# Kernel optimization log

Measured on AMD Instinct MI355X. Metric: run time of the kernel, lower is better.

## Reference

```python
import jax, jax.numpy as jnp
import numpy as np

CODEBOOK_SIZE = 1024
EMB_DIM = 64


def setup_inputs() -> dict:
    key = jax.random.key(0)
    k1, k2 = jax.random.split(key)
    z = jax.random.normal(k1, (4, EMB_DIM, 32, 32, 32), dtype=jnp.float32)
    embedding = jax.random.normal(k2, (CODEBOOK_SIZE, EMB_DIM), dtype=jnp.float32)
    return {"z": z, "embedding": embedding}


def reference(z, embedding):
    # z: [b, c, h, w, d], embedding: [K, c]
    b, c, h, w, d = z.shape
    K = embedding.shape[0]
    # flatten to [N, c] with channels last (matches permute(0,2,3,4,1).reshape)
    zf = jnp.transpose(z, (0, 2, 3, 4, 1)).reshape(-1, c)
    # squared L2 distance to each codebook entry: ||z||^2 - 2 z.e + ||e||^2
    dist = (
        jnp.sum(zf * zf, axis=1, keepdims=True)
        - 2.0 * zf @ embedding.T
        + jnp.sum(embedding * embedding, axis=1)[None, :]
    )  # [N, K]
    min_encoding_indices = jnp.argmin(dist, axis=1)  # [N]
    # one-hot @ embedding == gather (same math, no NxK materialization)
    z_q = embedding[min_encoding_indices]  # [N, c]
    z_q = jnp.transpose(z_q.reshape(b, h, w, d, c), (0, 4, 1, 2, 3))
    # straight-through estimator
    z_q = z + jax.lax.stop_gradient(z_q - z)
    # perplexity from mean one-hot occupancy
    n_tokens = zf.shape[0]
    e_mean = jnp.bincount(min_encoding_indices, length=K).astype(zf.dtype) / n_tokens
    perplexity = jnp.exp(-jnp.sum(e_mean * jnp.log(e_mean + 1e-10)))
    loss = jnp.asarray(0.0, dtype=z.dtype)
    return (
        z_q,
        loss,
        perplexity,
        min_encoding_indices.reshape(b, h, w, d),
        jnp.mean(dist),
    )
```

## Files before the change

kernel.cpp:

```cpp
#include <hip/hip_runtime.h>

#define CH     64
#define KC     1024
#define SP     32768
#define NBATCH 4
#define NTOK   (NBATCH * SP)
#define MTOK   64
#define SZZ    68
#define ECH    128
#define NCHK   (KC / ECH)
#define CAP    16
#define MARGIN 3.0f

#define OFF_ZQ   0
#define OFF_LOSS (NBATCH * CH * SP)
#define OFF_PERP (OFF_LOSS + 1)
#define OFF_IDX  (OFF_PERP + 1)
#define OFF_MEAN (OFF_IDX + NTOK)


typedef __attribute__((ext_vector_type(8))) short  s16x8;
typedef __attribute__((ext_vector_type(4))) float  f32x4;

__device__ __forceinline__ unsigned short f2bf(float f) {
    unsigned int u = __float_as_uint(f);
    return (unsigned short)((u + 0x7fffu + ((u >> 16) & 1u)) >> 16);
}

__device__ __forceinline__ float exact_dist(const float* zrow,
                                            const float* __restrict__ emb,
                                            const float* __restrict__ enl, int c) {
    const float4* er = (const float4*)(emb + (size_t)c * CH);
    float a0 = 0.f, a1 = 0.f, a2 = 0.f, a3 = 0.f;
#pragma unroll
    for (int j = 0; j < 16; ++j) {
        float4 e4 = er[j];
        a0 = fmaf(zrow[4 * j + 0], e4.x, a0);
        a1 = fmaf(zrow[4 * j + 1], e4.y, a1);
        a2 = fmaf(zrow[4 * j + 2], e4.z, a2);
        a3 = fmaf(zrow[4 * j + 3], e4.w, a3);
    }
    return enl[c] - 2.f * ((a0 + a1) + (a2 + a3));
}

__global__ __launch_bounds__(256) void prep(const float* __restrict__ e,
                                            int* __restrict__ hist,
                                            float* __restrict__ sums,
                                            float* __restrict__ sum_zc,
                                            float* __restrict__ sum_ec,
                                            float* __restrict__ enorm,
                                            unsigned short* __restrict__ eb) {
    const int tid = threadIdx.x;
    const int bk = blockIdx.x;
    if (bk < 4) {
        int k = bk * 256 + tid;
        const float4* row = (const float4*)(e + (size_t)k * CH);
        float n = 0.f;
#pragma unroll
        for (int j = 0; j < CH / 4; ++j) {
            float4 v = row[j];
            n += v.x * v.x + v.y * v.y + v.z * v.z + v.w * v.w;
        }
        enorm[k] = n;
    } else if (bk == 4) {
        if (tid == 0) sums[0] = 0.f;
        if (tid < 64) sum_zc[tid] = 0.f;
        __shared__ float ls1[256];
        __shared__ float r2[4];
        int c = tid & 63;
        int strip = tid >> 6;
        float s1 = 0.f, s2 = 0.f;
        for (int k = strip * 256; k < strip * 256 + 256; ++k) {
            float v = e[k * CH + c];
            s1 += v;
            s2 = fmaf(v, v, s2);
        }
        ls1[tid] = s1;
        for (int off = 32; off; off >>= 1) s2 += __shfl_down(s2, off);
        if ((tid & 63) == 0) r2[tid >> 6] = s2;
        __syncthreads();
        if (strip == 0) sum_ec[c] = ls1[c] + ls1[64 + c] + ls1[128 + c] + ls1[192 + c];
        if (tid == 0) sums[1] = r2[0] + r2[1] + r2[2] + r2[3];
    } else if (bk < 9) {
        hist[(bk - 5) * 256 + tid] = 0;
    } else {
        int base = (bk - 9) * 16384;
        for (int j = 0; j < 64; ++j) {
            int i = base + tid + j * 256;
            eb[i] = f2bf(e[i]);
        }
    }
}

#define GLD16(gsrc, ldst)                                                        \
    __builtin_amdgcn_global_load_lds(                                            \
        (const __attribute__((address_space(1))) unsigned int*)(gsrc),           \
        (__attribute__((address_space(3))) unsigned int*)(ldst), 16, 0, 0)

__global__ __launch_bounds__(256, 2) void vq_main(const float* __restrict__ z,
                                                  const float* __restrict__ emb,
                                                  const unsigned short* __restrict__ eb,
                                                  const float* __restrict__ enorm,
                                                  float* __restrict__ out,
                                                  int* __restrict__ hist,
                                                  float* __restrict__ sums,
                                                  float* __restrict__ sum_zc) {
    __shared__ float zl[MTOK * SZZ];
    __shared__ __align__(16) unsigned short ebl[ECH * 64];
    __shared__ float enl[ECH];
    __shared__ int   cand[MTOK][CAP];
    __shared__ int   ccnt[MTOK];
    __shared__ int   fi[MTOK];
    __shared__ float rbest[4][MTOK];
    __shared__ int   rbi[4][MTOK];

    const int tid = threadIdx.x;
    const int w = tid >> 6;
    const int lane = tid & 63;
    const int n15 = lane & 15;
    const int q = lane >> 4;
    const int t0 = blockIdx.x * MTOK;
    const int bb = t0 >> 15;
    const int s0 = t0 & (SP - 1);

    const int l3 = lane >> 3, l7 = lane & 7;
    const size_t gofs = (size_t)((l7 ^ l3) << 3);
#define STAGE(cb)                                                             \
    {                                                                         \
        _Pragma("unroll")                                                     \
        for (int it = 0; it < 4; ++it) {                                      \
            const unsigned short* gs =                                        \
                eb + (size_t)((cb) + (w << 5) + it * 8 + l3) * CH + gofs;     \
            GLD16(gs, (char*)ebl + (w << 12) + (it << 10));                   \
        }                                                                     \
    }

    {
        const float* zbase = z + ((size_t)bb * CH) * SP + s0;
#pragma unroll
        for (int j = 0; j < 4; ++j) {
            int idx = tid + j * 256;
            int c = idx >> 4;
            int tq = idx & 15;
            float4 v = *(const float4*)(zbase + (size_t)c * SP + tq * 4);
            zl[(4 * tq + 0) * SZZ + c] = v.x;
            zl[(4 * tq + 1) * SZZ + c] = v.y;
            zl[(4 * tq + 2) * SZZ + c] = v.z;
            zl[(4 * tq + 3) * SZZ + c] = v.w;
        }
        if (tid < MTOK) ccnt[tid] = 0;
    }
    __syncthreads();

    s16x8 A0, A1;
    {
        const float* zrow = &zl[(w * 16 + n15) * SZZ];
        float4 za = *(const float4*)(zrow + q * 8);
        float4 zb = *(const float4*)(zrow + q * 8 + 4);
        float4 zc = *(const float4*)(zrow + 32 + q * 8);
        float4 zd = *(const float4*)(zrow + 32 + q * 8 + 4);
        A0[0] = (short)f2bf(za.x); A0[1] = (short)f2bf(za.y);
        A0[2] = (short)f2bf(za.z); A0[3] = (short)f2bf(za.w);
        A0[4] = (short)f2bf(zb.x); A0[5] = (short)f2bf(zb.y);
        A0[6] = (short)f2bf(zb.z); A0[7] = (short)f2bf(zb.w);
        A1[0] = (short)f2bf(zc.x); A1[1] = (short)f2bf(zc.y);
        A1[2] = (short)f2bf(zc.z); A1[3] = (short)f2bf(zc.w);
        A1[4] = (short)f2bf(zd.x); A1[5] = (short)f2bf(zd.y);
        A1[6] = (short)f2bf(zd.z); A1[7] = (short)f2bf(zd.w);
    }
    const int gsw = q ^ (n15 & 7);

    float bmin[4] = {3.4e38f, 3.4e38f, 3.4e38f, 3.4e38f};
    for (int ch = 0; ch < NCHK; ++ch) {
        __syncthreads();
        STAGE(ch * ECH)
        if (tid < ECH) enl[tid] = enorm[ch * ECH + tid];
        __syncthreads();
        for (int ct = 0; ct < ECH / 16; ++ct) {
            const s16x8* rowp = (const s16x8*)&ebl[(size_t)(ct * 16 + n15) << 6];
            s16x8 B0 = rowp[gsw];
            s16x8 B1 = rowp[gsw ^ 4];
            f32x4 acc = {0.f, 0.f, 0.f, 0.f};
            acc = __builtin_amdgcn_mfma_f32_16x16x32_bf16(A0, B0, acc, 0, 0, 0);
            acc = __builtin_amdgcn_mfma_f32_16x16x32_bf16(A1, B1, acc, 0, 0, 0);
            float en = enl[ct * 16 + n15];
#pragma unroll
            for (int r = 0; r < 4; ++r) {
                float d = fmaf(-2.f, acc[r], en);
                bmin[r] = fminf(bmin[r], d);
            }
        }
    }
#pragma unroll
    for (int off = 1; off < 16; off <<= 1)
#pragma unroll
        for (int r = 0; r < 4; ++r)
            bmin[r] = fminf(bmin[r], __shfl_xor(bmin[r], off));
    float thr[4];
#pragma unroll
    for (int r = 0; r < 4; ++r) thr[r] = bmin[r] + MARGIN;

    for (int cc = 0; cc < NCHK; ++cc) {
        int ch = (cc == 0) ? (NCHK - 1) : (cc - 1);
        if (cc) {
            __syncthreads();
            STAGE(ch * ECH)
            if (tid < ECH) enl[tid] = enorm[ch * ECH + tid];
            __syncthreads();
        }
        for (int ct = 0; ct < ECH / 16; ++ct) {
            const s16x8* rowp = (const s16x8*)&ebl[(size_t)(ct * 16 + n15) << 6];
            s16x8 B0 = rowp[gsw];
            s16x8 B1 = rowp[gsw ^ 4];
            f32x4 acc = {0.f, 0.f, 0.f, 0.f};
            acc = __builtin_amdgcn_mfma_f32_16x16x32_bf16(A0, B0, acc, 0, 0, 0);
            acc = __builtin_amdgcn_mfma_f32_16x16x32_bf16(A1, B1, acc, 0, 0, 0);
            float en = enl[ct * 16 + n15];
#pragma unroll
            for (int r = 0; r < 4; ++r) {
                float d = fmaf(-2.f, acc[r], en);
                if (d <= thr[r]) {
                    int t = w * 16 + 4 * q + r;
                    int pos = atomicAdd(&ccnt[t], 1);
                    if (pos < CAP) cand[t][pos] = ch * ECH + ct * 16 + n15;
                }
            }
        }
    }
    __syncthreads();

    {
        const int t = tid & 63;
        const int part = tid >> 6;
        const float* zrow = &zl[t * SZZ];
        int cnt = ccnt[t];
        float best = 3.4e38f;
        int bi = 0;
        if (cnt <= CAP) {
            for (int j = part; j < cnt; j += 4) {
                int c = cand[t][j];
                float d = exact_dist(zrow, emb, enorm, c);
                if (d < best || (d == best && c < bi)) { best = d; bi = c; }
            }
        } else {
            for (int c = part; c < KC; c += 4) {
                float d = exact_dist(zrow, emb, enorm, c);
                if (d < best || (d == best && c < bi)) { best = d; bi = c; }
            }
        }
        rbest[part][t] = best;
        rbi[part][t] = bi;
    }
    __syncthreads();
    if (tid < MTOK) {
        float best = rbest[0][tid];
        int bi = rbi[0][tid];
#pragma unroll
        for (int p = 1; p < 4; ++p) {
            float b = rbest[p][tid];
            int i = rbi[p][tid];
            if (b < best || (b == best && i < bi)) { best = b; bi = i; }
        }
        fi[tid] = bi;
        out[OFF_IDX + t0 + tid] = (float)bi;
        atomicAdd(&hist[bi], 1);
    }
    __syncthreads();

#pragma unroll
    for (int j = 0; j < 16; ++j) {
        int idx = tid + j * 256;
        int c = idx >> 6;
        int t = idx & 63;
        int code = fi[t];
        float ev = emb[(size_t)code * CH + c];
        float zv = zl[t * SZZ + c];
        out[OFF_ZQ + ((size_t)bb * CH + c) * SP + s0 + t] = zv + (ev - zv);
    }

    {
        float* zs1 = reinterpret_cast<float*>(cand);
        float* zs2 = zs1 + 256;
        int c = tid >> 2, qq = tid & 3;
        float s1 = 0.f, s2 = 0.f;
        for (int tt = 0; tt < 16; ++tt) {
            float v = zl[(qq * 16 + tt) * SZZ + c];
            s1 += v;
            s2 = fmaf(v, v, s2);
        }
        zs1[tid] = s1;
        zs2[tid] = s2;
        __syncthreads();
        if (tid < 64) {
            float a = zs1[4 * tid] + zs1[4 * tid + 1] + zs1[4 * tid + 2] + zs1[4 * tid + 3];
            atomicAdd(&sum_zc[tid], a);
            float bsum = zs2[4 * tid] + zs2[4 * tid + 1] + zs2[4 * tid + 2] + zs2[4 * tid + 3];
            for (int off = 32; off; off >>= 1) bsum += __shfl_down(bsum, off);
            if (tid == 0) atomicAdd(&sums[0], bsum);
        }
    }
#undef STAGE
}

__global__ __launch_bounds__(1024) void finalize(const int* __restrict__ hist,
                                                 const float* __restrict__ sums,
                                                 const float* __restrict__ sum_zc,
                                                 const float* __restrict__ sum_ec,
                                                 float* __restrict__ out) {
    __shared__ float red[1024];
    int k = threadIdx.x;
    float p = (float)hist[k] * (1.0f / (float)NTOK);
    red[k] = p * logf(p + 1e-10f);
    __syncthreads();
    for (int off = 512; off; off >>= 1) {
        if (k < off) red[k] += red[k + off];
        __syncthreads();
    }
    if (k == 0) {
        out[OFF_PERP] = expf(-red[0]);
        out[OFF_LOSS] = 0.f;
        double dot = 0.0;
        for (int c = 0; c < CH; ++c) dot += (double)sum_zc[c] * (double)sum_ec[c];
        double mean = ((double)KC * (double)sums[0] + (double)NTOK * (double)sums[1] - 2.0 * dot)
                      / ((double)NTOK * (double)KC);
        out[OFF_MEAN] = (float)mean;
    }
}

extern "C" void kernel_launch(void* const* d_in, const int* in_sizes, int n_in,
                              void* d_out, int out_size, void* d_ws, size_t ws_size,
                              hipStream_t stream) {
    const float* z   = (const float*)d_in[0];
    const float* emb = (const float*)d_in[1];
    float* out = (float*)d_out;

    int*            hist   = (int*)d_ws;
    float*          sums   = (float*)d_ws + 1024;
    float*          sum_zc = (float*)d_ws + 1026;
    float*          sum_ec = (float*)d_ws + 1090;
    float*          enorm  = (float*)d_ws + 1154;
    unsigned short* eb     = (unsigned short*)((int*)d_ws + 4096);

    prep<<<13, 256, 0, stream>>>(emb, hist, sums, sum_zc, sum_ec, enorm, eb);
    vq_main<<<NTOK / MTOK, 256, 0, stream>>>(z, emb, eb, enorm, out, hist, sums, sum_zc);
    finalize<<<1, 1024, 0, stream>>>(hist, sums, sum_zc, sum_ec, out);
}
```

Before: 209.8 us.

## Split codebook columns across waves, each wave covering all 64 tokens

Before, each wave held one 16-token A fragment and swept all 128 codes of each staged chunk. Now each wave holds A fragments for all 64 tokens and handles only its own 32-code slice, so every B fragment read from LDS feeds four MFMA pairs. Per-wave minima are merged through shared memory with an extra barrier to form the thresholds. This trades more A registers and a cross-wave reduction for fewer LDS B reads per MFMA.

```diff
diff --git a/kernel.cpp b/kernel.cpp
--- a/kernel.cpp
+++ b/kernel.cpp
@@ -96,6 +96,16 @@
     __builtin_amdgcn_global_load_lds(                                            \
         (const __attribute__((address_space(1))) unsigned int*)(gsrc),           \
         (__attribute__((address_space(3))) unsigned int*)(ldst), 16, 0, 0)
+
+#define MK8(A, ptr)                                            \
+    {                                                          \
+        float4 _a = *(const float4*)(ptr);                     \
+        float4 _b = *(const float4*)((ptr) + 4);               \
+        A[0] = (short)f2bf(_a.x); A[1] = (short)f2bf(_a.y);    \
+        A[2] = (short)f2bf(_a.z); A[3] = (short)f2bf(_a.w);    \
+        A[4] = (short)f2bf(_b.x); A[5] = (short)f2bf(_b.y);    \
+        A[6] = (short)f2bf(_b.z); A[7] = (short)f2bf(_b.w);    \
+    }
 
 __global__ __launch_bounds__(256, 2) void vq_main(const float* __restrict__ z,
                                                   const float* __restrict__ emb,
@@ -152,53 +162,85 @@
     }
     __syncthreads();
 
-    s16x8 A0, A1;
+    s16x8 A00, A01, A10, A11, A20, A21, A30, A31;
     {
-        const float* zrow = &zl[(w * 16 + n15) * SZZ];
-        float4 za = *(const float4*)(zrow + q * 8);
-        float4 zb = *(const float4*)(zrow + q * 8 + 4);
-        float4 zc = *(const float4*)(zrow + 32 + q * 8);
-        float4 zd = *(const float4*)(zrow + 32 + q * 8 + 4);
-        A0[0] = (short)f2bf(za.x); A0[1] = (short)f2bf(za.y);
-        A0[2] = (short)f2bf(za.z); A0[3] = (short)f2bf(za.w);
-        A0[4] = (short)f2bf(zb.x); A0[5] = (short)f2bf(zb.y);
-        A0[6] = (short)f2bf(zb.z); A0[7] = (short)f2bf(zb.w);
-        A1[0] = (short)f2bf(zc.x); A1[1] = (short)f2bf(zc.y);
-        A1[2] = (short)f2bf(zc.z); A1[3] = (short)f2bf(zc.w);
-        A1[4] = (short)f2bf(zd.x); A1[5] = (short)f2bf(zd.y);
-        A1[6] = (short)f2bf(zd.z); A1[7] = (short)f2bf(zd.w);
+        const float* zr0 = &zl[(0 * 16 + n15) * SZZ];
+        const float* zr1 = &zl[(1 * 16 + n15) * SZZ];
+        const float* zr2 = &zl[(2 * 16 + n15) * SZZ];
+        const float* zr3 = &zl[(3 * 16 + n15) * SZZ];
+        MK8(A00, zr0 + q * 8) MK8(A01, zr0 + 32 + q * 8)
+        MK8(A10, zr1 + q * 8) MK8(A11, zr1 + 32 + q * 8)
+        MK8(A20, zr2 + q * 8) MK8(A21, zr2 + 32 + q * 8)
+        MK8(A30, zr3 + q * 8) MK8(A31, zr3 + 32 + q * 8)
     }
     const int gsw = q ^ (n15 & 7);
 
-    float bmin[4] = {3.4e38f, 3.4e38f, 3.4e38f, 3.4e38f};
+    float bm0[4] = {3.4e38f, 3.4e38f, 3.4e38f, 3.4e38f};
+    float bm1[4] = {3.4e38f, 3.4e38f, 3.4e38f, 3.4e38f};
+    float bm2[4] = {3.4e38f, 3.4e38f, 3.4e38f, 3.4e38f};
+    float bm3[4] = {3.4e38f, 3.4e38f, 3.4e38f, 3.4e38f};
     for (int ch = 0; ch < NCHK; ++ch) {
         __syncthreads();
         STAGE(ch * ECH)
         if (tid < ECH) enl[tid] = enorm[ch * ECH + tid];
         __syncthreads();
-        for (int ct = 0; ct < ECH / 16; ++ct) {
-            const s16x8* rowp = (const s16x8*)&ebl[(size_t)(ct * 16 + n15) << 6];
+#pragma unroll
+        for (int ct = 0; ct < 2; ++ct) {
+            const int row = (w << 5) + ct * 16 + n15;
+            const s16x8* rowp = (const s16x8*)&ebl[(size_t)row << 6];
             s16x8 B0 = rowp[gsw];
             s16x8 B1 = rowp[gsw ^ 4];
-            f32x4 acc = {0.f, 0.f, 0.f, 0.f};
-            acc = __builtin_amdgcn_mfma_f32_16x16x32_bf16(A0, B0, acc, 0, 0, 0);
-            acc = __builtin_amdgcn_mfma_f32_16x16x32_bf16(A1, B1, acc, 0, 0, 0);
-            float en = enl[ct * 16 + n15];
+            float en = enl[row];
+            f32x4 a0 = {0.f, 0.f, 0.f, 0.f};
+            f32x4 a1 = {0.f, 0.f, 0.f, 0.f};
+            f32x4 a2 = {0.f, 0.f, 0.f, 0.f};
+            f32x4 a3 = {0.f, 0.f, 0.f, 0.f};
+            a0 = __builtin_amdgcn_mfma_f32_16x16x32_bf16(A00, B0, a0, 0, 0, 0);
+            a0 = __builtin_amdgcn_mfma_f32_16x16x32_bf16(A01, B1, a0, 0, 0, 0);
+            a1 = __builtin_amdgcn_mfma_f32_16x16x32_bf16(A10, B0, a1, 0, 0, 0);
+            a1 = __builtin_amdgcn_mfma_f32_16x16x32_bf16(A11, B1, a1, 0, 0, 0);
+            a2 = __builtin_amdgcn_mfma_f32_16x16x32_bf16(A20, B0, a2, 0, 0, 0);
+            a2 = __builtin_amdgcn_mfma_f32_16x16x32_bf16(A21, B1, a2, 0, 0, 0);
+            a3 = __builtin_amdgcn_mfma_f32_16x16x32_bf16(A30, B0, a3, 0, 0, 0);
+            a3 = __builtin_amdgcn_mfma_f32_16x16x32_bf16(A31, B1, a3, 0, 0, 0);
 #pragma unroll
             for (int r = 0; r < 4; ++r) {
-                float d = fmaf(-2.f, acc[r], en);
-                bmin[r] = fminf(bmin[r], d);
+                bm0[r] = fminf(bm0[r], fmaf(-2.f, a0[r], en));
+                bm1[r] = fminf(bm1[r], fmaf(-2.f, a1[r], en));
+                bm2[r] = fminf(bm2[r], fmaf(-2.f, a2[r], en));
+                bm3[r] = fminf(bm3[r], fmaf(-2.f, a3[r], en));
             }
         }
     }
 #pragma unroll
     for (int off = 1; off < 16; off <<= 1)
 #pragma unroll
-        for (int r = 0; r < 4; ++r)
-            bmin[r] = fminf(bmin[r], __shfl_xor(bmin[r], off));
-    float thr[4];
-#pragma unroll
-    for (int r = 0; r < 4; ++r) thr[r] = bmin[r] + MARGIN;
+        for (int r = 0; r < 4; ++r) {
+            bm0[r] = fminf(bm0[r], __shfl_xor(bm0[r], off));
+            bm1[r] = fminf(bm1[r], __shfl_xor(bm1[r], off));
+            bm2[r] = fminf(bm2[r], __shfl_xor(bm2[r], off));
+            bm3[r] = fminf(bm3[r], __shfl_xor(bm3[r], off));
+        }
+    float* wmin = &rbest[0][0];
+    if (n15 == 0) {
+#pragma unroll
+        for (int r = 0; r < 4; ++r) {
+            wmin[w * 64 + 0 + 4 * q + r]  = bm0[r];
+            wmin[w * 64 + 16 + 4 * q + r] = bm1[r];
+            wmin[w * 64 + 32 + 4 * q + r] = bm2[r];
+            wmin[w * 64 + 48 + 4 * q + r] = bm3[r];
+        }
+    }
+    __syncthreads();
+    float thr0[4], thr1[4], thr2[4], thr3[4];
+#pragma unroll
+    for (int r = 0; r < 4; ++r) {
+        int i0 = 0 + 4 * q + r, i1 = 16 + 4 * q + r, i2 = 32 + 4 * q + r, i3 = 48 + 4 * q + r;
+        thr0[r] = fminf(fminf(wmin[i0], wmin[64 + i0]), fminf(wmin[128 + i0], wmin[192 + i0])) + MARGIN;
+        thr1[r] = fminf(fminf(wmin[i1], wmin[64 + i1]), fminf(wmin[128 + i1], wmin[192 + i1])) + MARGIN;
+        thr2[r] = fminf(fminf(wmin[i2], wmin[64 + i2]), fminf(wmin[128 + i2], wmin[192 + i2])) + MARGIN;
+        thr3[r] = fminf(fminf(wmin[i3], wmin[64 + i3]), fminf(wmin[128 + i3], wmin[192 + i3])) + MARGIN;
+    }
 
     for (int cc = 0; cc < NCHK; ++cc) {
         int ch = (cc == 0) ? (NCHK - 1) : (cc - 1);
@@ -208,21 +250,51 @@
             if (tid < ECH) enl[tid] = enorm[ch * ECH + tid];
             __syncthreads();
         }
-        for (int ct = 0; ct < ECH / 16; ++ct) {
-            const s16x8* rowp = (const s16x8*)&ebl[(size_t)(ct * 16 + n15) << 6];
+#pragma unroll
+        for (int ct = 0; ct < 2; ++ct) {
+            const int row = (w << 5) + ct * 16 + n15;
+            const s16x8* rowp = (const s16x8*)&ebl[(size_t)row << 6];
             s16x8 B0 = rowp[gsw];
             s16x8 B1 = rowp[gsw ^ 4];
-            f32x4 acc = {0.f, 0.f, 0.f, 0.f};
-            acc = __builtin_amdgcn_mfma_f32_16x16x32_bf16(A0, B0, acc, 0, 0, 0);
-            acc = __builtin_amdgcn_mfma_f32_16x16x32_bf16(A1, B1, acc, 0, 0, 0);
-            float en = enl[ct * 16 + n15];
+            float en = enl[row];
+            f32x4 a0 = {0.f, 0.f, 0.f, 0.f};
+            f32x4 a1 = {0.f, 0.f, 0.f, 0.f};
+            f32x4 a2 = {0.f, 0.f, 0.f, 0.f};
+            f32x4 a3 = {0.f, 0.f, 0.f, 0.f};
+            a0 = __builtin_amdgcn_mfma_f32_16x16x32_bf16(A00, B0, a0, 0, 0, 0);
+            a0 = __builtin_amdgcn_mfma_f32_16x16x32_bf16(A01, B1, a0, 0, 0, 0);
+            a1 = __builtin_amdgcn_mfma_f32_16x16x32_bf16(A10, B0, a1, 0, 0, 0);
+            a1 = __builtin_amdgcn_mfma_f32_16x16x32_bf16(A11, B1, a1, 0, 0, 0);
+            a2 = __builtin_amdgcn_mfma_f32_16x16x32_bf16(A20, B0, a2, 0, 0, 0);
+            a2 = __builtin_amdgcn_mfma_f32_16x16x32_bf16(A21, B1, a2, 0, 0, 0);
+            a3 = __builtin_amdgcn_mfma_f32_16x16x32_bf16(A30, B0, a3, 0, 0, 0);
+            a3 = __builtin_amdgcn_mfma_f32_16x16x32_bf16(A31, B1, a3, 0, 0, 0);
+            int code = ch * ECH + row;
 #pragma unroll
             for (int r = 0; r < 4; ++r) {
-                float d = fmaf(-2.f, acc[r], en);
-                if (d <= thr[r]) {
-                    int t = w * 16 + 4 * q + r;
+                float d0 = fmaf(-2.f, a0[r], en);
+                if (d0 <= thr0[r]) {
+                    int t = 0 + 4 * q + r;
                     int pos = atomicAdd(&ccnt[t], 1);
-                    if (pos < CAP) cand[t][pos] = ch * ECH + ct * 16 + n15;
+                    if (pos < CAP) cand[t][pos] = code;
+                }
+                float d1 = fmaf(-2.f, a1[r], en);
+                if (d1 <= thr1[r]) {
+                    int t = 16 + 4 * q + r;
+                    int pos = atomicAdd(&ccnt[t], 1);
+                    if (pos < CAP) cand[t][pos] = code;
+                }
+                float d2 = fmaf(-2.f, a2[r], en);
+                if (d2 <= thr2[r]) {
+                    int t = 32 + 4 * q + r;
+                    int pos = atomicAdd(&ccnt[t], 1);
+                    if (pos < CAP) cand[t][pos] = code;
+                }
+                float d3 = fmaf(-2.f, a3[r], en);
+                if (d3 <= thr3[r]) {
+                    int t = 48 + 4 * q + r;
+                    int pos = atomicAdd(&ccnt[t], 1);
+                    if (pos < CAP) cand[t][pos] = code;
                 }
             }
         }
```

Result: no change. 212.5 us (+1.3%).

## Double-buffer codebook chunk staging to overlap loads with MFMA compute

Applied to the files above, without the earlier changes.

Shrinks each codebook chunk from 128 to 64 entries and splits the LDS staging buffers into two halves. The next chunk's async global-to-LDS copy and norm load are issued before the current chunk is computed, in both the min-distance pass and the candidate pass. This hides global-load latency behind the MFMA work and cuts the barriers per chunk from two to one. The trade-off is twice as many chunk iterations, and correctness now depends on the barrier also waiting for the outstanding LDS-DMA loads.

```diff
diff --git a/kernel.cpp b/kernel.cpp
--- a/kernel.cpp
+++ b/kernel.cpp
@@ -7,7 +7,7 @@
 #define NTOK   (NBATCH * SP)
 #define MTOK   64
 #define SZZ    68
-#define ECH    128
+#define ECH    64
 #define NCHK   (KC / ECH)
 #define CAP    16
 #define MARGIN 3.0f
@@ -106,8 +106,8 @@
                                                   float* __restrict__ sums,
                                                   float* __restrict__ sum_zc) {
     __shared__ float zl[MTOK * SZZ];
-    __shared__ __align__(16) unsigned short ebl[ECH * 64];
-    __shared__ float enl[ECH];
+    __shared__ __align__(16) unsigned short ebl[2][ECH * 64];
+    __shared__ float enl[2][ECH];
     __shared__ int   cand[MTOK][CAP];
     __shared__ int   ccnt[MTOK];
     __shared__ int   fi[MTOK];
@@ -125,13 +125,13 @@
 
     const int l3 = lane >> 3, l7 = lane & 7;
     const size_t gofs = (size_t)((l7 ^ l3) << 3);
-#define STAGE(cb)                                                             \
+#define STAGE(cb, b)                                                          \
     {                                                                         \
         _Pragma("unroll")                                                     \
-        for (int it = 0; it < 4; ++it) {                                      \
+        for (int it = 0; it < 2; ++it) {                                      \
             const unsigned short* gs =                                        \
-                eb + (size_t)((cb) + (w << 5) + it * 8 + l3) * CH + gofs;     \
-            GLD16(gs, (char*)ebl + (w << 12) + (it << 10));                   \
+                eb + (size_t)((cb) + (w << 4) + it * 8 + l3) * CH + gofs;     \
+            GLD16(gs, (char*)ebl + (b) * 8192 + (w << 11) + (it << 10));      \
         }                                                                     \
     }
 
@@ -149,6 +149,8 @@
             zl[(4 * tq + 3) * SZZ + c] = v.w;
         }
         if (tid < MTOK) ccnt[tid] = 0;
+        STAGE(0, 0)
+        if (tid < ECH) enl[0][tid] = enorm[tid];
     }
     __syncthreads();
 
@@ -171,25 +173,29 @@
     const int gsw = q ^ (n15 & 7);
 
     float bmin[4] = {3.4e38f, 3.4e38f, 3.4e38f, 3.4e38f};
+    int buf = 0;
     for (int ch = 0; ch < NCHK; ++ch) {
-        __syncthreads();
-        STAGE(ch * ECH)
-        if (tid < ECH) enl[tid] = enorm[ch * ECH + tid];
-        __syncthreads();
+        if (ch < NCHK - 1) {
+            STAGE((ch + 1) * ECH, buf ^ 1)
+            if (tid < ECH) enl[buf ^ 1][tid] = enorm[(ch + 1) * ECH + tid];
+        }
+#pragma unroll
         for (int ct = 0; ct < ECH / 16; ++ct) {
-            const s16x8* rowp = (const s16x8*)&ebl[(size_t)(ct * 16 + n15) << 6];
+            const s16x8* rowp = (const s16x8*)&ebl[buf][(size_t)(ct * 16 + n15) << 6];
             s16x8 B0 = rowp[gsw];
             s16x8 B1 = rowp[gsw ^ 4];
             f32x4 acc = {0.f, 0.f, 0.f, 0.f};
             acc = __builtin_amdgcn_mfma_f32_16x16x32_bf16(A0, B0, acc, 0, 0, 0);
             acc = __builtin_amdgcn_mfma_f32_16x16x32_bf16(A1, B1, acc, 0, 0, 0);
-            float en = enl[ct * 16 + n15];
+            float en = enl[buf][ct * 16 + n15];
 #pragma unroll
             for (int r = 0; r < 4; ++r) {
                 float d = fmaf(-2.f, acc[r], en);
                 bmin[r] = fminf(bmin[r], d);
             }
         }
+        __syncthreads();
+        if (ch < NCHK - 1) buf ^= 1;
     }
 #pragma unroll
     for (int off = 1; off < 16; off <<= 1)
@@ -201,21 +207,20 @@
     for (int r = 0; r < 4; ++r) thr[r] = bmin[r] + MARGIN;
 
     for (int cc = 0; cc < NCHK; ++cc) {
-        int ch = (cc == 0) ? (NCHK - 1) : (cc - 1);
-        if (cc) {
-            __syncthreads();
-            STAGE(ch * ECH)
-            if (tid < ECH) enl[tid] = enorm[ch * ECH + tid];
-            __syncthreads();
-        }
+        const int ch = (cc == 0) ? (NCHK - 1) : (cc - 1);
+        if (cc < NCHK - 1) {
+            STAGE(cc * ECH, buf ^ 1)
+            if (tid < ECH) enl[buf ^ 1][tid] = enorm[cc * ECH + tid];
+        }
+#pragma unroll
         for (int ct = 0; ct < ECH / 16; ++ct) {
-            const s16x8* rowp = (const s16x8*)&ebl[(size_t)(ct * 16 + n15) << 6];
+            const s16x8* rowp = (const s16x8*)&ebl[buf][(size_t)(ct * 16 + n15) << 6];
             s16x8 B0 = rowp[gsw];
             s16x8 B1 = rowp[gsw ^ 4];
             f32x4 acc = {0.f, 0.f, 0.f, 0.f};
             acc = __builtin_amdgcn_mfma_f32_16x16x32_bf16(A0, B0, acc, 0, 0, 0);
             acc = __builtin_amdgcn_mfma_f32_16x16x32_bf16(A1, B1, acc, 0, 0, 0);
-            float en = enl[ct * 16 + n15];
+            float en = enl[buf][ct * 16 + n15];
 #pragma unroll
             for (int r = 0; r < 4; ++r) {
                 float d = fmaf(-2.f, acc[r], en);
@@ -226,8 +231,9 @@
                 }
             }
         }
-    }
-    __syncthreads();
+        __syncthreads();
+        if (cc < NCHK - 1) buf ^= 1;
+    }
 
     {
         const int t = tid & 63;
```

After: 218.2 us. +4.0%, slower.

## Keep whole bf16 codebook resident in LDS with persistent blocks over token tiles

Applied to the files above, without the earlier changes.

The kernel becomes persistent: 256 blocks each load the full 1024x64 bf16 codebook and the norms into about 159 KB of dynamic shared memory once, then loop over 8 token tiles. This removes the per-tile restaging of codebook chunks and the many barriers that went with each chunk, and the second pass no longer reloads chunks. In exchange occupancy falls to one 4-wave block per CU, so there is no overlap between global z loads, MFMA work and the refinement phase.

```diff
diff --git a/kernel.cpp b/kernel.cpp
--- a/kernel.cpp
+++ b/kernel.cpp
@@ -7,10 +7,20 @@
 #define NTOK   (NBATCH * SP)
 #define MTOK   64
 #define SZZ    68
-#define ECH    128
-#define NCHK   (KC / ECH)
+#define NBLK   256
+#define TILES  (NTOK / MTOK / NBLK)
 #define CAP    16
 #define MARGIN 3.0f
+
+#define OFF_EBL   0
+#define OFF_ZL    131072
+#define OFF_ENL   148480
+#define OFF_RBEST 152576
+#define OFF_RBI   153600
+#define OFF_CAND  154624
+#define OFF_CCNT  158720
+#define OFF_FI    158976
+#define SMEM_BYTES 159232
 
 #define OFF_ZQ   0
 #define OFF_LOSS (NBATCH * CH * SP)
@@ -97,86 +107,84 @@
         (const __attribute__((address_space(1))) unsigned int*)(gsrc),           \
         (__attribute__((address_space(3))) unsigned int*)(ldst), 16, 0, 0)
 
-__global__ __launch_bounds__(256, 2) void vq_main(const float* __restrict__ z,
-                                                  const float* __restrict__ emb,
-                                                  const unsigned short* __restrict__ eb,
-                                                  const float* __restrict__ enorm,
-                                                  float* __restrict__ out,
-                                                  int* __restrict__ hist,
-                                                  float* __restrict__ sums,
-                                                  float* __restrict__ sum_zc) {
-    __shared__ float zl[MTOK * SZZ];
-    __shared__ __align__(16) unsigned short ebl[ECH * 64];
-    __shared__ float enl[ECH];
-    __shared__ int   cand[MTOK][CAP];
-    __shared__ int   ccnt[MTOK];
-    __shared__ int   fi[MTOK];
-    __shared__ float rbest[4][MTOK];
-    __shared__ int   rbi[4][MTOK];
+__global__ __launch_bounds__(256) void vq_main(const float* __restrict__ z,
+                                               const float* __restrict__ emb,
+                                               const unsigned short* __restrict__ eb,
+                                               const float* __restrict__ enorm,
+                                               float* __restrict__ out,
+                                               int* __restrict__ hist,
+                                               float* __restrict__ sums,
+                                               float* __restrict__ sum_zc) {
+    extern __shared__ __align__(16) char smem[];
+    unsigned short* ebl = (unsigned short*)(smem + OFF_EBL);
+    float* zl   = (float*)(smem + OFF_ZL);
+    float* enl  = (float*)(smem + OFF_ENL);
+    float* rbest = (float*)(smem + OFF_RBEST);
+    int*   rbi   = (int*)(smem + OFF_RBI);
+    int (*cand)[CAP] = (int (*)[CAP])(smem + OFF_CAND);
+    int*   ccnt = (int*)(smem + OFF_CCNT);
+    int*   fi   = (int*)(smem + OFF_FI);
 
     const int tid = threadIdx.x;
     const int w = tid >> 6;
     const int lane = tid & 63;
     const int n15 = lane & 15;
     const int q = lane >> 4;
-    const int t0 = blockIdx.x * MTOK;
-    const int bb = t0 >> 15;
-    const int s0 = t0 & (SP - 1);
-
-    const int l3 = lane >> 3, l7 = lane & 7;
-    const size_t gofs = (size_t)((l7 ^ l3) << 3);
-#define STAGE(cb)                                                             \
-    {                                                                         \
-        _Pragma("unroll")                                                     \
-        for (int it = 0; it < 4; ++it) {                                      \
-            const unsigned short* gs =                                        \
-                eb + (size_t)((cb) + (w << 5) + it * 8 + l3) * CH + gofs;     \
-            GLD16(gs, (char*)ebl + (w << 12) + (it << 10));                   \
-        }                                                                     \
-    }
+    const int gsw = q ^ (n15 & 7);
 
     {
-        const float* zbase = z + ((size_t)bb * CH) * SP + s0;
-#pragma unroll
-        for (int j = 0; j < 4; ++j) {
-            int idx = tid + j * 256;
-            int c = idx >> 4;
-            int tq = idx & 15;
-            float4 v = *(const float4*)(zbase + (size_t)c * SP + tq * 4);
-            zl[(4 * tq + 0) * SZZ + c] = v.x;
-            zl[(4 * tq + 1) * SZZ + c] = v.y;
-            zl[(4 * tq + 2) * SZZ + c] = v.z;
-            zl[(4 * tq + 3) * SZZ + c] = v.w;
-        }
-        if (tid < MTOK) ccnt[tid] = 0;
-    }
-    __syncthreads();
-
-    s16x8 A0, A1;
-    {
-        const float* zrow = &zl[(w * 16 + n15) * SZZ];
-        float4 za = *(const float4*)(zrow + q * 8);
-        float4 zb = *(const float4*)(zrow + q * 8 + 4);
-        float4 zc = *(const float4*)(zrow + 32 + q * 8);
-        float4 zd = *(const float4*)(zrow + 32 + q * 8 + 4);
-        A0[0] = (short)f2bf(za.x); A0[1] = (short)f2bf(za.y);
-        A0[2] = (short)f2bf(za.z); A0[3] = (short)f2bf(za.w);
-        A0[4] = (short)f2bf(zb.x); A0[5] = (short)f2bf(zb.y);
-        A0[6] = (short)f2bf(zb.z); A0[7] = (short)f2bf(zb.w);
-        A1[0] = (short)f2bf(zc.x); A1[1] = (short)f2bf(zc.y);
-        A1[2] = (short)f2bf(zc.z); A1[3] = (short)f2bf(zc.w);
-        A1[4] = (short)f2bf(zd.x); A1[5] = (short)f2bf(zd.y);
-        A1[6] = (short)f2bf(zd.z); A1[7] = (short)f2bf(zd.w);
-    }
-    const int gsw = q ^ (n15 & 7);
-
-    float bmin[4] = {3.4e38f, 3.4e38f, 3.4e38f, 3.4e38f};
-    for (int ch = 0; ch < NCHK; ++ch) {
-        __syncthreads();
-        STAGE(ch * ECH)
-        if (tid < ECH) enl[tid] = enorm[ch * ECH + tid];
-        __syncthreads();
-        for (int ct = 0; ct < ECH / 16; ++ct) {
+        const int l3 = lane >> 3, l7 = lane & 7;
+        const size_t gofs = (size_t)((l7 ^ l3) << 3);
+        for (int it = 0; it < 32; ++it) {
+            const unsigned short* gs =
+                eb + (size_t)((w << 8) + it * 8 + l3) * CH + gofs;
+            GLD16(gs, (char*)ebl + (w << 15) + (it << 10));
+        }
+#pragma unroll
+        for (int j = 0; j < 4; ++j) enl[tid + j * 256] = enorm[tid + j * 256];
+    }
+
+    for (int tile = 0; tile < TILES; ++tile) {
+        const int t0 = (blockIdx.x + (tile << 8)) * MTOK;
+        const int bb = t0 >> 15;
+        const int s0 = t0 & (SP - 1);
+
+        {
+            const float* zbase = z + ((size_t)bb * CH) * SP + s0;
+#pragma unroll
+            for (int j = 0; j < 4; ++j) {
+                int idx = tid + j * 256;
+                int c = idx >> 4;
+                int tq = idx & 15;
+                float4 v = *(const float4*)(zbase + (size_t)c * SP + tq * 4);
+                zl[(4 * tq + 0) * SZZ + c] = v.x;
+                zl[(4 * tq + 1) * SZZ + c] = v.y;
+                zl[(4 * tq + 2) * SZZ + c] = v.z;
+                zl[(4 * tq + 3) * SZZ + c] = v.w;
+            }
+            if (tid < MTOK) ccnt[tid] = 0;
+        }
+        __syncthreads();
+
+        s16x8 A0, A1;
+        {
+            const float* zrow = &zl[(w * 16 + n15) * SZZ];
+            float4 za = *(const float4*)(zrow + q * 8);
+            float4 zb = *(const float4*)(zrow + q * 8 + 4);
+            float4 zc = *(const float4*)(zrow + 32 + q * 8);
+            float4 zd = *(const float4*)(zrow + 32 + q * 8 + 4);
+            A0[0] = (short)f2bf(za.x); A0[1] = (short)f2bf(za.y);
+            A0[2] = (short)f2bf(za.z); A0[3] = (short)f2bf(za.w);
+            A0[4] = (short)f2bf(zb.x); A0[5] = (short)f2bf(zb.y);
+            A0[6] = (short)f2bf(zb.z); A0[7] = (short)f2bf(zb.w);
+            A1[0] = (short)f2bf(zc.x); A1[1] = (short)f2bf(zc.y);
+            A1[2] = (short)f2bf(zc.z); A1[3] = (short)f2bf(zc.w);
+            A1[4] = (short)f2bf(zd.x); A1[5] = (short)f2bf(zd.y);
+            A1[6] = (short)f2bf(zd.z); A1[7] = (short)f2bf(zd.w);
+        }
+
+        float bmin[4] = {3.4e38f, 3.4e38f, 3.4e38f, 3.4e38f};
+        for (int ct = 0; ct < KC / 16; ++ct) {
             const s16x8* rowp = (const s16x8*)&ebl[(size_t)(ct * 16 + n15) << 6];
             s16x8 B0 = rowp[gsw];
             s16x8 B1 = rowp[gsw ^ 4];
@@ -190,25 +198,16 @@
                 bmin[r] = fminf(bmin[r], d);
             }
         }
-    }
-#pragma unroll
-    for (int off = 1; off < 16; off <<= 1)
-#pragma unroll
-        for (int r = 0; r < 4; ++r)
-            bmin[r] = fminf(bmin[r], __shfl_xor(bmin[r], off));
-    float thr[4];
-#pragma unroll
-    for (int r = 0; r < 4; ++r) thr[r] = bmin[r] + MARGIN;
-
-    for (int cc = 0; cc < NCHK; ++cc) {
-        int ch = (cc == 0) ? (NCHK - 1) : (cc - 1);
-        if (cc) {
-            __syncthreads();
-            STAGE(ch * ECH)
-            if (tid < ECH) enl[tid] = enorm[ch * ECH + tid];
-            __syncthreads();
-        }
-        for (int ct = 0; ct < ECH / 16; ++ct) {
+#pragma unroll
+        for (int off = 1; off < 16; off <<= 1)
+#pragma unroll
+            for (int r = 0; r < 4; ++r)
+                bmin[r] = fminf(bmin[r], __shfl_xor(bmin[r], off));
+        float thr[4];
+#pragma unroll
+        for (int r = 0; r < 4; ++r) thr[r] = bmin[r] + MARGIN;
+
+        for (int ct = 0; ct < KC / 16; ++ct) {
             const s16x8* rowp = (const s16x8*)&ebl[(size_t)(ct * 16 + n15) << 6];
             s16x8 B0 = rowp[gsw];
             s16x8 B1 = rowp[gsw ^ 4];
@@ -216,90 +215,91 @@
             acc = __builtin_amdgcn_mfma_f32_16x16x32_bf16(A0, B0, acc, 0, 0, 0);
             acc = __builtin_amdgcn_mfma_f32_16x16x32_bf16(A1, B1, acc, 0, 0, 0);
             float en = enl[ct * 16 + n15];
+            int code = ct * 16 + n15;
 #pragma unroll
             for (int r = 0; r < 4; ++r) {
                 float d = fmaf(-2.f, acc[r], en);
                 if (d <= thr[r]) {
                     int t = w * 16 + 4 * q + r;
                     int pos = atomicAdd(&ccnt[t], 1);
-                    if (pos < CAP) cand[t][pos] = ch * ECH + ct * 16 + n15;
+                    if (pos < CAP) cand[t][pos] = code;
                 }
             }
         }
-    }
-    __syncthreads();
-
-    {
-        const int t = tid & 63;
-        const int part = tid >> 6;
-        const float* zrow = &zl[t * SZZ];
-        int cnt = ccnt[t];
-        float best = 3.4e38f;
-        int bi = 0;
-        if (cnt <= CAP) {
-            for (int j = part; j < cnt; j += 4) {
-                int c = cand[t][j];
-                float d = exact_dist(zrow, emb, enorm, c);
-                if (d < best || (d == best && c < bi)) { best = d; bi = c; }
-            }
-        } else {
-            for (int c = part; c < KC; c += 4) {
-                float d = exact_dist(zrow, emb, enorm, c);
-                if (d < best || (d == best && c < bi)) { best = d; bi = c; }
-            }
-        }
-        rbest[part][t] = best;
-        rbi[part][t] = bi;
-    }
-    __syncthreads();
-    if (tid < MTOK) {
-        float best = rbest[0][tid];
-        int bi = rbi[0][tid];
-#pragma unroll
-        for (int p = 1; p < 4; ++p) {
-            float b = rbest[p][tid];
-            int i = rbi[p][tid];
-            if (b < best || (b == best && i < bi)) { best = b; bi = i; }
-        }
-        fi[tid] = bi;
-        out[OFF_IDX + t0 + tid] = (float)bi;
-        atomicAdd(&hist[bi], 1);
-    }
-    __syncthreads();
-
-#pragma unroll
-    for (int j = 0; j < 16; ++j) {
-        int idx = tid + j * 256;
-        int c = idx >> 6;
-        int t = idx & 63;
-        int code = fi[t];
-        float ev = emb[(size_t)code * CH + c];
-        float zv = zl[t * SZZ + c];
-        out[OFF_ZQ + ((size_t)bb * CH + c) * SP + s0 + t] = zv + (ev - zv);
-    }
-
-    {
-        float* zs1 = reinterpret_cast<float*>(cand);
-        float* zs2 = zs1 + 256;
-        int c = tid >> 2, qq = tid & 3;
-        float s1 = 0.f, s2 = 0.f;
-        for (int tt = 0; tt < 16; ++tt) {
-            float v = zl[(qq * 16 + tt) * SZZ + c];
-            s1 += v;
-            s2 = fmaf(v, v, s2);
-        }
-        zs1[tid] = s1;
-        zs2[tid] = s2;
-        __syncthreads();
-        if (tid < 64) {
-            float a = zs1[4 * tid] + zs1[4 * tid + 1] + zs1[4 * tid + 2] + zs1[4 * tid + 3];
-            atomicAdd(&sum_zc[tid], a);
-            float bsum = zs2[4 * tid] + zs2[4 * tid + 1] + zs2[4 * tid + 2] + zs2[4 * tid + 3];
-            for (int off = 32; off; off >>= 1) bsum += __shfl_down(bsum, off);
-            if (tid == 0) atomicAdd(&sums[0], bsum);
-        }
-    }
-#undef STAGE
+        __syncthreads();
+
+        {
+            const int t = tid & 63;
+            const int part = tid >> 6;
+            const float* zrow = &zl[t * SZZ];
+            int cnt = ccnt[t];
+            float best = 3.4e38f;
+            int bi = 0;
+            if (cnt <= CAP) {
+                for (int j = part; j < cnt; j += 4) {
+                    int c = cand[t][j];
+                    float d = exact_dist(zrow, emb, enl, c);
+                    if (d < best || (d == best && c < bi)) { best = d; bi = c; }
+                }
+            } else {
+                for (int c = part; c < KC; c += 4) {
+                    float d = exact_dist(zrow, emb, enl, c);
+                    if (d < best || (d == best && c < bi)) { best = d; bi = c; }
+                }
+            }
+            rbest[part * MTOK + t] = best;
+            rbi[part * MTOK + t] = bi;
+        }
+        __syncthreads();
+        if (tid < MTOK) {
+            float best = rbest[tid];
+            int bi = rbi[tid];
+#pragma unroll
+            for (int p = 1; p < 4; ++p) {
+                float b = rbest[p * MTOK + tid];
+                int i = rbi[p * MTOK + tid];
+                if (b < best || (b == best && i < bi)) { best = b; bi = i; }
+            }
+            fi[tid] = bi;
+            out[OFF_IDX + t0 + tid] = (float)bi;
+            atomicAdd(&hist[bi], 1);
+        }
+        __syncthreads();
+
+#pragma unroll
+        for (int j = 0; j < 16; ++j) {
+            int idx = tid + j * 256;
+            int c = idx >> 6;
+            int t = idx & 63;
+            int code = fi[t];
+            float ev = emb[(size_t)code * CH + c];
+            float zv = zl[t * SZZ + c];
+            out[OFF_ZQ + ((size_t)bb * CH + c) * SP + s0 + t] = zv + (ev - zv);
+        }
+
+        {
+            float* zs1 = reinterpret_cast<float*>(cand);
+            float* zs2 = zs1 + 256;
+            int c = tid >> 2, qq = tid & 3;
+            float s1 = 0.f, s2 = 0.f;
+            for (int tt = 0; tt < 16; ++tt) {
+                float v = zl[(qq * 16 + tt) * SZZ + c];
+                s1 += v;
+                s2 = fmaf(v, v, s2);
+            }
+            zs1[tid] = s1;
+            zs2[tid] = s2;
+            __syncthreads();
+            if (tid < 64) {
+                float a = zs1[4 * tid] + zs1[4 * tid + 1] + zs1[4 * tid + 2] + zs1[4 * tid + 3];
+                atomicAdd(&sum_zc[tid], a);
+                float bsum = zs2[4 * tid] + zs2[4 * tid + 1] + zs2[4 * tid + 2] + zs2[4 * tid + 3];
+                for (int off = 32; off; off >>= 1) bsum += __shfl_down(bsum, off);
+                if (tid == 0) atomicAdd(&sums[0], bsum);
+            }
+        }
+        __syncthreads();
+    }
 }
 
 __global__ __launch_bounds__(1024) void finalize(const int* __restrict__ hist,
@@ -341,7 +341,10 @@
     float*          enorm  = (float*)d_ws + 1154;
     unsigned short* eb     = (unsigned short*)((int*)d_ws + 4096);
 
+    hipFuncSetAttribute(reinterpret_cast<const void*>(&vq_main),
+                        hipFuncAttributeMaxDynamicSharedMemorySize, SMEM_BYTES);
+
     prep<<<13, 256, 0, stream>>>(emb, hist, sums, sum_zc, sum_ec, enorm, eb);
-    vq_main<<<NTOK / MTOK, 256, 0, stream>>>(z, emb, eb, enorm, out, hist, sums, sum_zc);
+    vq_main<<<NBLK, 256, SMEM_BYTES, stream>>>(z, emb, eb, enorm, out, hist, sums, sum_zc);
     finalize<<<1, 1024, 0, stream>>>(hist, sums, sum_zc, sum_ec, out);
 }
```

Result: slower. 290.6 us (+38.5%).
